# Kernel tuning notes

Hardware: AMD Instinct MI355X
Metric: run time of the kernel (lower is better)

## Reference

```python
import jax, jax.numpy as jnp
import numpy as np
import math

DIM = 512
B, T, H, W = 1, 8, 64, 64


def setup_inputs() -> dict:
    key = jax.random.key(0)
    k0, k1, k2 = jax.random.split(key, 3)
    x = jax.random.normal(k0, (B, DIM, T, H, W), dtype=jnp.float32)
    gamma = jnp.ones((DIM,), jnp.float32)                      # RMS_norm gamma (viewed as flat vector)
    w_qkv = jax.random.normal(k1, (3 * DIM, DIM), jnp.float32) * 0.02  # conv1x1 weight (out, in)
    b_qkv = jnp.zeros((3 * DIM,), jnp.float32)
    w_proj = jax.random.normal(k2, (DIM, DIM), jnp.float32) * 0.02     # zero-init in torch; random for a meaningful baseline
    b_proj = jnp.zeros((DIM,), jnp.float32)
    return dict(x=x, gamma=gamma, w_qkv=w_qkv, b_qkv=b_qkv, w_proj=w_proj, b_proj=b_proj)


def reference(x, gamma, w_qkv, b_qkv, w_proj, b_proj):
    b, c, t, h, w = x.shape
    xt = jnp.transpose(x, (0, 2, 3, 4, 1))          # [b, t, h, w, c]
    identity = xt
    y = xt.reshape(b * t, h, w, c)
    # RMS_norm: L2 norm over channels (last dim), clamped, scaled by sqrt(c)*gamma
    norm = jnp.clip(jnp.linalg.norm(y, axis=-1, keepdims=True), 1e-12, None)
    y = y / norm * (c ** 0.5) * gamma
    # 1x1 conv QKV as GEMM over channels
    qkv = jnp.einsum('bhwc,oc->bhwo', y, w_qkv) + b_qkv        # [bt, h, w, 3c]
    qkv = qkv.reshape(b * t, h * w, 1, 3 * c)                  # nh=1 per source rearrange
    q, k, v = jnp.split(qkv, 3, axis=-1)                       # each [bt, hw, 1, c]
    scale = 1.0 / math.sqrt(c)
    # NOTE: hw sits in the batch position (faithful to source); seq len = nh = 1
    attn = jnp.einsum('bsnc,bsmc->bsnm', q, k) * scale         # [bt, hw, 1, 1]
    attn = jax.nn.softmax(attn, axis=-1)                       # trivially 1.0
    o = jnp.einsum('bsnm,bsmc->bsnc', attn, v)                 # == v
    o = o.reshape(b * t, h, w, c)
    o = jnp.einsum('bhwc,oc->bhwo', o, w_proj) + b_proj        # 1x1 proj conv
    o = o.reshape(b, t, h, w, c)
    out = jnp.transpose(o + identity, (0, 4, 1, 2, 3))         # back to [b, c, t, h, w]
    return out
```

## Files before the change

### kernel.cpp

```cpp
#include <hip/hip_runtime.h>

typedef unsigned short ushort_t;
typedef __attribute__((ext_vector_type(8))) short short8;
typedef __attribute__((ext_vector_type(4))) float f32x4;

#define DIMC 512
#define PN   32768
#define SQRTC 22.627416997969522f

__device__ __forceinline__ ushort_t f2bf(float f) {
  unsigned int u = __float_as_uint(f);
  unsigned int r = u + 0x7fffu + ((u >> 16) & 1u);
  return (ushort_t)(r >> 16);
}

__global__ __launch_bounds__(256) void k_cast(const float* __restrict__ a,
                                              ushort_t* __restrict__ b) {
  int i = (blockIdx.x * 256 + threadIdx.x) * 4;
  float4 v = *(const float4*)(a + i);
  ushort_t o[4] = {f2bf(v.x), f2bf(v.y), f2bf(v.z), f2bf(v.w)};
  *(uint2*)(b + i) = *(const uint2*)o;
}

__global__ __launch_bounds__(64) void k_wvt(const float* __restrict__ wqkv,
                                            ushort_t* __restrict__ WvT) {
  int c = blockIdx.x;
  int k8 = threadIdx.x * 8;
  ushort_t tmp[8];
#pragma unroll
  for (int j = 0; j < 8; ++j)
    tmp[j] = f2bf(wqkv[(long)(1024 + k8 + j) * DIMC + c]);
  *(uint4*)(WvT + (long)c * DIMC + k8) = *(const uint4*)tmp;
}

__global__ __launch_bounds__(256) void k_fb(const float* __restrict__ wp,
                                            const float* __restrict__ bqkv,
                                            const float* __restrict__ bproj,
                                            float* __restrict__ fb) {
  int wave = threadIdx.x >> 6;
  int lane = threadIdx.x & 63;
  int o = blockIdx.x * 4 + wave;
  float part = 0.f;
#pragma unroll
  for (int i = 0; i < 8; ++i) {
    int k = lane + i * 64;
    part += wp[o * DIMC + k] * bqkv[1024 + k];
  }
  for (int off = 32; off; off >>= 1) part += __shfl_down(part, off, 64);
  if (lane == 0) fb[o] = part + bproj[o];
}

__global__ __launch_bounds__(256) void k_prep_x(const float* __restrict__ x,
                                                ushort_t* __restrict__ xT,
                                                float* __restrict__ s) {
  __shared__ ushort_t xt[64 * 264];
  __shared__ float red[16 * 64];
  int tid = threadIdx.x;
  long p0 = (long)blockIdx.x * 64;
  int cg = tid >> 4;
  int p4 = (tid & 15) * 4;
  float ss0 = 0.f, ss1 = 0.f, ss2 = 0.f, ss3 = 0.f;
  for (int half = 0; half < 2; ++half) {
    __syncthreads();
#pragma unroll 4
    for (int pass = 0; pass < 16; ++pass) {
      int cl = pass * 16 + cg;
      int c = half * 256 + cl;
      float4 v = *(const float4*)(x + (long)c * PN + p0 + p4);
      xt[(p4 + 0) * 264 + cl] = f2bf(v.x);
      xt[(p4 + 1) * 264 + cl] = f2bf(v.y);
      xt[(p4 + 2) * 264 + cl] = f2bf(v.z);
      xt[(p4 + 3) * 264 + cl] = f2bf(v.w);
      ss0 += v.x * v.x; ss1 += v.y * v.y; ss2 += v.z * v.z; ss3 += v.w * v.w;
    }
    __syncthreads();
#pragma unroll
    for (int i = 0; i < 8; ++i) {
      int chunk = tid + i * 256;
      int r = chunk >> 5;
      int c8 = (chunk & 31) * 8;
      uint4 v = *(const uint4*)(&xt[r * 264 + c8]);
      *(uint4*)(xT + (p0 + r) * DIMC + half * 256 + c8) = v;
    }
  }
  red[cg * 64 + p4 + 0] = ss0;
  red[cg * 64 + p4 + 1] = ss1;
  red[cg * 64 + p4 + 2] = ss2;
  red[cg * 64 + p4 + 3] = ss3;
  __syncthreads();
  if (tid < 64) {
    float t = 0.f;
#pragma unroll
    for (int g = 0; g < 16; ++g) t += red[g * 64 + tid];
    s[p0 + tid] = SQRTC / fmaxf(sqrtf(t), 1e-12f);
  }
}

template <int EPI>
__global__ __launch_bounds__(256) void k_gemm_f(
    const ushort_t* __restrict__ A,
    const ushort_t* __restrict__ BT,
    long Nstr,
    void* __restrict__ Cv,
    const float* __restrict__ gamma,
    const float* __restrict__ xid,
    const float* __restrict__ fb,
    const float* __restrict__ s) {
  __shared__ ushort_t As[128 * 64];
  __shared__ ushort_t Bs[128 * 64];
  int tid = threadIdx.x;
  int p0 = blockIdx.x * 128;
  int o0 = blockIdx.y * 128;
  int wave = tid >> 6, lane = tid & 63;
  int wo = (wave & 1) * 64, wp = (wave >> 1) * 64;
  int q = lane >> 4, ln = lane & 15;

  f32x4 zero = {0.f, 0.f, 0.f, 0.f};
  f32x4 acc[4][4];
#pragma unroll
  for (int i = 0; i < 4; ++i)
#pragma unroll
    for (int j = 0; j < 4; ++j) acc[i][j] = zero;

  int sr = tid >> 3;
  int sc = tid & 7;
  const ushort_t* Ag = A + (long)(o0 + sr) * DIMC + sc * 8;
  const ushort_t* Bg = BT + (long)(p0 + sr) * DIMC + sc * 8;

  for (int kc = 0; kc < DIMC; kc += 64) {
    __syncthreads();
#pragma unroll
    for (int it = 0; it < 4; ++it) {
      int r = sr + it * 32;
      uint4 va = *(const uint4*)(Ag + (long)it * 32 * DIMC + kc);
      uint4 vb = *(const uint4*)(Bg + (long)it * 32 * DIMC + kc);
      int sw = ((sc ^ (r & 7)) * 8);
      *(uint4*)(&As[r * 64 + sw]) = va;
      *(uint4*)(&Bs[r * 64 + sw]) = vb;
    }
    __syncthreads();
#pragma unroll
    for (int ks = 0; ks < 2; ++ks) {
      int cch = ks * 4 + q;
      short8 af[4], bf[4];
#pragma unroll
      for (int mi = 0; mi < 4; ++mi) {
        int row = wo + mi * 16 + ln;
        af[mi] = *(const short8*)(&As[row * 64 + ((cch ^ (row & 7)) * 8)]);
      }
#pragma unroll
      for (int ni = 0; ni < 4; ++ni) {
        int row = wp + ni * 16 + ln;
        bf[ni] = *(const short8*)(&Bs[row * 64 + ((cch ^ (row & 7)) * 8)]);
      }
#pragma unroll
      for (int mi = 0; mi < 4; ++mi)
#pragma unroll
        for (int ni = 0; ni < 4; ++ni)
          acc[mi][ni] = __builtin_amdgcn_mfma_f32_16x16x32_bf16(af[mi], bf[ni], acc[mi][ni], 0, 0, 0);
    }
  }

#pragma unroll
  for (int mi = 0; mi < 4; ++mi) {
    int obase = o0 + wo + mi * 16 + q * 4;
#pragma unroll
    for (int ni = 0; ni < 4; ++ni) {
      int p = p0 + wp + ni * 16 + ln;
      if (EPI == 0) {
        ushort_t* C = (ushort_t*)Cv;
        float g = gamma[p];
#pragma unroll
        for (int r = 0; r < 4; ++r)
          C[(long)(obase + r) * Nstr + p] = f2bf(acc[mi][ni][r] * g);
      } else {
        float* C = (float*)Cv;
        float sv = s[p];
#pragma unroll
        for (int r = 0; r < 4; ++r) {
          int o = obase + r;
          C[(long)o * Nstr + p] = xid[(long)o * Nstr + p] + fb[o] + sv * acc[mi][ni][r];
        }
      }
    }
  }
}

extern "C" void kernel_launch(void* const* d_in, const int* in_sizes, int n_in,
                              void* d_out, int out_size, void* d_ws, size_t ws_size,
                              hipStream_t stream) {
  const float* x     = (const float*)d_in[0];
  const float* gamma = (const float*)d_in[1];
  const float* wqkv  = (const float*)d_in[2];
  const float* bqkv  = (const float*)d_in[3];
  const float* wproj = (const float*)d_in[4];
  const float* bproj = (const float*)d_in[5];

  char* ws = (char*)d_ws;
  ushort_t* Mp  = (ushort_t*)(ws);
  ushort_t* wpb = (ushort_t*)(ws + 524288);
  ushort_t* WvT = (ushort_t*)(ws + 1048576);
  float*    fb  = (float*)(ws + 1572864);
  float*    s   = (float*)(ws + 1576960);
  ushort_t* xT  = (ushort_t*)(ws + 2097152);

  k_cast<<<dim3(256), dim3(256), 0, stream>>>(wproj, wpb);
  k_wvt<<<dim3(512), dim3(64), 0, stream>>>(wqkv, WvT);
  k_fb<<<dim3(128), dim3(256), 0, stream>>>(wproj, bqkv, bproj, fb);
  k_prep_x<<<dim3(512), dim3(256), 0, stream>>>(x, xT, s);
  k_gemm_f<0><<<dim3(4, 4), dim3(256), 0, stream>>>(
      wpb, WvT, 512, Mp, gamma, nullptr, nullptr, nullptr);
  k_gemm_f<1><<<dim3(256, 4), dim3(256), 0, stream>>>(
      Mp, xT, PN, d_out, nullptr, x, fb, s);
}
```

Before: 176.6 us.

## Merge prep kernels into one launch, use direct global-to-LDS loads, vectorize epilogue

Combines the weight cast, Wv transpose, bias fold, x transpose/norm and the small weight GEMM into one heterogeneous kernel that branches on block index. This cuts the six launches down to two. The main GEMM now loads tiles with global_load_lds, writing swizzled rows straight into shared memory. Its epilogue is staged through LDS so the residual read and output write use float4 along the pixel dimension instead of scalar strided stores. In exchange, the small GEMM reads its B operand from LDS with scalar gathers, and the epilogue adds extra block-wide barriers.

```diff
diff --git a/kernel.cpp b/kernel.cpp
--- a/kernel.cpp
+++ b/kernel.cpp
@@ -13,101 +13,169 @@
   unsigned int r = u + 0x7fffu + ((u >> 16) & 1u);
   return (ushort_t)(r >> 16);
 }
-
-__global__ __launch_bounds__(256) void k_cast(const float* __restrict__ a,
-                                              ushort_t* __restrict__ b) {
-  int i = (blockIdx.x * 256 + threadIdx.x) * 4;
-  float4 v = *(const float4*)(a + i);
-  ushort_t o[4] = {f2bf(v.x), f2bf(v.y), f2bf(v.z), f2bf(v.w)};
-  *(uint2*)(b + i) = *(const uint2*)o;
-}
-
-__global__ __launch_bounds__(64) void k_wvt(const float* __restrict__ wqkv,
-                                            ushort_t* __restrict__ WvT) {
-  int c = blockIdx.x;
-  int k8 = threadIdx.x * 8;
-  ushort_t tmp[8];
-#pragma unroll
-  for (int j = 0; j < 8; ++j)
-    tmp[j] = f2bf(wqkv[(long)(1024 + k8 + j) * DIMC + c]);
-  *(uint4*)(WvT + (long)c * DIMC + k8) = *(const uint4*)tmp;
-}
-
-__global__ __launch_bounds__(256) void k_fb(const float* __restrict__ wp,
-                                            const float* __restrict__ bqkv,
-                                            const float* __restrict__ bproj,
-                                            float* __restrict__ fb) {
-  int wave = threadIdx.x >> 6;
-  int lane = threadIdx.x & 63;
-  int o = blockIdx.x * 4 + wave;
-  float part = 0.f;
-#pragma unroll
-  for (int i = 0; i < 8; ++i) {
-    int k = lane + i * 64;
-    part += wp[o * DIMC + k] * bqkv[1024 + k];
+__device__ __forceinline__ unsigned int pack2(float lo, float hi) {
+  return ((unsigned int)f2bf(hi) << 16) | (unsigned int)f2bf(lo);
+}
+
+typedef __attribute__((address_space(1))) unsigned int glb_u32;
+typedef __attribute__((address_space(3))) unsigned int lds_u32;
+__device__ __forceinline__ void gl_lds16(const ushort_t* g, ushort_t* l) {
+  __builtin_amdgcn_global_load_lds((const glb_u32*)(g), (lds_u32*)(l), 16, 0, 0);
+}
+
+__global__ __launch_bounds__(256) void k_prep(
+    const float* __restrict__ x, const float* __restrict__ gamma,
+    const float* __restrict__ wqkv, const float* __restrict__ bqkv,
+    const float* __restrict__ wproj, const float* __restrict__ bproj,
+    ushort_t* __restrict__ Mp, float* __restrict__ fb,
+    float* __restrict__ s, ushort_t* __restrict__ xT) {
+  __shared__ ushort_t uls[18944];
+  int bb = blockIdx.x;
+  int tid = threadIdx.x;
+
+  if (bb < 512) {
+    ushort_t* xt = uls;
+    float* red = (float*)(uls + 16896);
+    long p0 = (long)bb * 64;
+    int cg = tid >> 4;
+    int p4 = (tid & 15) * 4;
+    float ss0 = 0.f, ss1 = 0.f, ss2 = 0.f, ss3 = 0.f;
+    for (int half = 0; half < 2; ++half) {
+      __syncthreads();
+#pragma unroll 4
+      for (int pass = 0; pass < 16; ++pass) {
+        int cl = pass * 16 + cg;
+        int c = half * 256 + cl;
+        float4 v = *(const float4*)(x + (long)c * PN + p0 + p4);
+        xt[(p4 + 0) * 264 + cl] = f2bf(v.x);
+        xt[(p4 + 1) * 264 + cl] = f2bf(v.y);
+        xt[(p4 + 2) * 264 + cl] = f2bf(v.z);
+        xt[(p4 + 3) * 264 + cl] = f2bf(v.w);
+        ss0 += v.x * v.x; ss1 += v.y * v.y; ss2 += v.z * v.z; ss3 += v.w * v.w;
+      }
+      __syncthreads();
+#pragma unroll
+      for (int i = 0; i < 8; ++i) {
+        int chunk = tid + i * 256;
+        int r = chunk >> 5;
+        int c8 = (chunk & 31) * 8;
+        uint4 v = *(const uint4*)(&xt[r * 264 + c8]);
+        *(uint4*)(xT + (p0 + r) * DIMC + half * 256 + c8) = v;
+      }
+    }
+    red[cg * 64 + p4 + 0] = ss0;
+    red[cg * 64 + p4 + 1] = ss1;
+    red[cg * 64 + p4 + 2] = ss2;
+    red[cg * 64 + p4 + 3] = ss3;
+    __syncthreads();
+    if (tid < 64) {
+      float t = 0.f;
+#pragma unroll
+      for (int g = 0; g < 16; ++g) t += red[g * 64 + tid];
+      s[p0 + tid] = SQRTC / fmaxf(sqrtf(t), 1e-12f);
+    }
+
+  } else if (bb < 528) {
+    ushort_t* As = uls;
+    ushort_t* Bs = uls + 8192;
+    const float* A = wproj;
+    const float* B = wqkv + 1024 * DIMC;
+    int bidx = bb - 512;
+    int p0 = (bidx & 3) * 128;
+    int o0 = (bidx >> 2) * 128;
+    int wave = tid >> 6, lane = tid & 63;
+    int wo = (wave & 1) * 64, wp = (wave >> 1) * 64;
+    int q = lane >> 4, ln = lane & 15;
+    f32x4 zero = {0.f, 0.f, 0.f, 0.f};
+    f32x4 acc[4][4];
+#pragma unroll
+    for (int i = 0; i < 4; ++i)
+#pragma unroll
+      for (int j = 0; j < 4; ++j) acc[i][j] = zero;
+    int ar = tid >> 3, ac = (tid & 7) * 8;
+    int br = tid >> 4, bc = (tid & 15) * 8;
+    for (int kc = 0; kc < DIMC; kc += 64) {
+      __syncthreads();
+#pragma unroll
+      for (int it = 0; it < 4; ++it) {
+        int r = ar + it * 32;
+        const float* ap = A + (long)(o0 + r) * DIMC + kc + ac;
+        float4 a0 = *(const float4*)ap;
+        float4 a1 = *(const float4*)(ap + 4);
+        uint4 wa;
+        wa.x = pack2(a0.x, a0.y); wa.y = pack2(a0.z, a0.w);
+        wa.z = pack2(a1.x, a1.y); wa.w = pack2(a1.z, a1.w);
+        *(uint4*)(&As[r * 64 + ac]) = wa;
+        int kr = br + it * 16;
+        const float* bp = B + (long)(kc + kr) * DIMC + p0 + bc;
+        float4 b0 = *(const float4*)bp;
+        float4 b1 = *(const float4*)(bp + 4);
+        uint4 wb;
+        wb.x = pack2(b0.x, b0.y); wb.y = pack2(b0.z, b0.w);
+        wb.z = pack2(b1.x, b1.y); wb.w = pack2(b1.z, b1.w);
+        *(uint4*)(&Bs[kr * 128 + bc]) = wb;
+      }
+      __syncthreads();
+#pragma unroll
+      for (int ks = 0; ks < 2; ++ks) {
+        int kb = ks * 32 + q * 8;
+        short8 af[4], bfr[4];
+#pragma unroll
+        for (int mi = 0; mi < 4; ++mi)
+          af[mi] = *(const short8*)(&As[(wo + mi * 16 + ln) * 64 + kb]);
+#pragma unroll
+        for (int ni = 0; ni < 4; ++ni) {
+          int pl = wp + ni * 16 + ln;
+          short8 t;
+#pragma unroll
+          for (int j = 0; j < 8; ++j) t[j] = (short)Bs[(kb + j) * 128 + pl];
+          bfr[ni] = t;
+        }
+#pragma unroll
+        for (int mi = 0; mi < 4; ++mi)
+#pragma unroll
+          for (int ni = 0; ni < 4; ++ni)
+            acc[mi][ni] = __builtin_amdgcn_mfma_f32_16x16x32_bf16(af[mi], bfr[ni], acc[mi][ni], 0, 0, 0);
+      }
+    }
+#pragma unroll
+    for (int mi = 0; mi < 4; ++mi) {
+      int obase = o0 + wo + mi * 16 + q * 4;
+#pragma unroll
+      for (int ni = 0; ni < 4; ++ni) {
+        int p = p0 + wp + ni * 16 + ln;
+        float g = gamma[p];
+#pragma unroll
+        for (int r = 0; r < 4; ++r)
+          Mp[(long)(obase + r) * DIMC + p] = f2bf(acc[mi][ni][r] * g);
+      }
+    }
+
+  } else {
+    int wave = tid >> 6;
+    int lane = tid & 63;
+    int o = (bb - 528) * 4 + wave;
+    float part = 0.f;
+#pragma unroll
+    for (int i = 0; i < 8; ++i) {
+      int k = lane + i * 64;
+      part += wproj[o * DIMC + k] * bqkv[1024 + k];
+    }
+    for (int off = 32; off; off >>= 1) part += __shfl_down(part, off, 64);
+    if (lane == 0) fb[o] = part + bproj[o];
   }
-  for (int off = 32; off; off >>= 1) part += __shfl_down(part, off, 64);
-  if (lane == 0) fb[o] = part + bproj[o];
-}
-
-__global__ __launch_bounds__(256) void k_prep_x(const float* __restrict__ x,
-                                                ushort_t* __restrict__ xT,
-                                                float* __restrict__ s) {
-  __shared__ ushort_t xt[64 * 264];
-  __shared__ float red[16 * 64];
-  int tid = threadIdx.x;
-  long p0 = (long)blockIdx.x * 64;
-  int cg = tid >> 4;
-  int p4 = (tid & 15) * 4;
-  float ss0 = 0.f, ss1 = 0.f, ss2 = 0.f, ss3 = 0.f;
-  for (int half = 0; half < 2; ++half) {
-    __syncthreads();
-#pragma unroll 4
-    for (int pass = 0; pass < 16; ++pass) {
-      int cl = pass * 16 + cg;
-      int c = half * 256 + cl;
-      float4 v = *(const float4*)(x + (long)c * PN + p0 + p4);
-      xt[(p4 + 0) * 264 + cl] = f2bf(v.x);
-      xt[(p4 + 1) * 264 + cl] = f2bf(v.y);
-      xt[(p4 + 2) * 264 + cl] = f2bf(v.z);
-      xt[(p4 + 3) * 264 + cl] = f2bf(v.w);
-      ss0 += v.x * v.x; ss1 += v.y * v.y; ss2 += v.z * v.z; ss3 += v.w * v.w;
-    }
-    __syncthreads();
-#pragma unroll
-    for (int i = 0; i < 8; ++i) {
-      int chunk = tid + i * 256;
-      int r = chunk >> 5;
-      int c8 = (chunk & 31) * 8;
-      uint4 v = *(const uint4*)(&xt[r * 264 + c8]);
-      *(uint4*)(xT + (p0 + r) * DIMC + half * 256 + c8) = v;
-    }
-  }
-  red[cg * 64 + p4 + 0] = ss0;
-  red[cg * 64 + p4 + 1] = ss1;
-  red[cg * 64 + p4 + 2] = ss2;
-  red[cg * 64 + p4 + 3] = ss3;
-  __syncthreads();
-  if (tid < 64) {
-    float t = 0.f;
-#pragma unroll
-    for (int g = 0; g < 16; ++g) t += red[g * 64 + tid];
-    s[p0 + tid] = SQRTC / fmaxf(sqrtf(t), 1e-12f);
-  }
-}
-
-template <int EPI>
-__global__ __launch_bounds__(256) void k_gemm_f(
+}
+
+__global__ __launch_bounds__(256) void k_main(
     const ushort_t* __restrict__ A,
     const ushort_t* __restrict__ BT,
-    long Nstr,
-    void* __restrict__ Cv,
-    const float* __restrict__ gamma,
+    float* __restrict__ C,
     const float* __restrict__ xid,
     const float* __restrict__ fb,
     const float* __restrict__ s) {
-  __shared__ ushort_t As[128 * 64];
-  __shared__ ushort_t Bs[128 * 64];
+  __shared__ ushort_t smem[2 * 128 * 64];
+  ushort_t* As = smem;
+  ushort_t* Bs = smem + 128 * 64;
   int tid = threadIdx.x;
   int p0 = blockIdx.x * 128;
   int o0 = blockIdx.y * 128;
@@ -122,22 +190,19 @@
 #pragma unroll
     for (int j = 0; j < 4; ++j) acc[i][j] = zero;
 
-  int sr = tid >> 3;
-  int sc = tid & 7;
-  const ushort_t* Ag = A + (long)(o0 + sr) * DIMC + sc * 8;
-  const ushort_t* Bg = BT + (long)(p0 + sr) * DIMC + sc * 8;
+  int lr = lane >> 3;
+  int lc = lane & 7;
+  int csw = lc ^ lr;
 
   for (int kc = 0; kc < DIMC; kc += 64) {
     __syncthreads();
 #pragma unroll
     for (int it = 0; it < 4; ++it) {
-      int r = sr + it * 32;
-      uint4 va = *(const uint4*)(Ag + (long)it * 32 * DIMC + kc);
-      uint4 vb = *(const uint4*)(Bg + (long)it * 32 * DIMC + kc);
-      int sw = ((sc ^ (r & 7)) * 8);
-      *(uint4*)(&As[r * 64 + sw]) = va;
-      *(uint4*)(&Bs[r * 64 + sw]) = vb;
-    }
+      int rb = (it * 4 + wave) * 8;
+      gl_lds16(A  + (long)(o0 + rb + lr) * DIMC + kc + csw * 8, &As[rb * 64]);
+      gl_lds16(BT + (long)(p0 + rb + lr) * DIMC + kc + csw * 8, &Bs[rb * 64]);
+    }
+    asm volatile("s_waitcnt vmcnt(0)" ::: "memory");
     __syncthreads();
 #pragma unroll
     for (int ks = 0; ks < 2; ++ks) {
@@ -161,27 +226,31 @@
     }
   }
 
+  float* scr = (float*)smem + wave * 1088;
+  float4 s4 = *(const float4*)(s + p0 + wp + ln * 4);
 #pragma unroll
   for (int mi = 0; mi < 4; ++mi) {
-    int obase = o0 + wo + mi * 16 + q * 4;
-#pragma unroll
-    for (int ni = 0; ni < 4; ++ni) {
-      int p = p0 + wp + ni * 16 + ln;
-      if (EPI == 0) {
-        ushort_t* C = (ushort_t*)Cv;
-        float g = gamma[p];
-#pragma unroll
-        for (int r = 0; r < 4; ++r)
-          C[(long)(obase + r) * Nstr + p] = f2bf(acc[mi][ni][r] * g);
-      } else {
-        float* C = (float*)Cv;
-        float sv = s[p];
-#pragma unroll
-        for (int r = 0; r < 4; ++r) {
-          int o = obase + r;
-          C[(long)o * Nstr + p] = xid[(long)o * Nstr + p] + fb[o] + sv * acc[mi][ni][r];
-        }
-      }
+    __syncthreads();
+#pragma unroll
+    for (int ni = 0; ni < 4; ++ni)
+#pragma unroll
+      for (int r = 0; r < 4; ++r)
+        scr[(q * 4 + r) * 68 + ni * 16 + ln] = acc[mi][ni][r];
+    __syncthreads();
+    int ob = o0 + wo + mi * 16 + q;
+    int p = p0 + wp + ln * 4;
+#pragma unroll
+    for (int j = 0; j < 4; ++j) {
+      int o = ob + j * 4;
+      float4 d = *(const float4*)(&scr[(q + j * 4) * 68 + ln * 4]);
+      float4 xv = *(const float4*)(xid + (long)o * PN + p);
+      float fbv = fb[o];
+      float4 ov;
+      ov.x = xv.x + fbv + s4.x * d.x;
+      ov.y = xv.y + fbv + s4.y * d.y;
+      ov.z = xv.z + fbv + s4.z * d.z;
+      ov.w = xv.w + fbv + s4.w * d.w;
+      *(float4*)(C + (long)o * PN + p) = ov;
     }
   }
 }
@@ -197,19 +266,12 @@
   const float* bproj = (const float*)d_in[5];
 
   char* ws = (char*)d_ws;
-  ushort_t* Mp  = (ushort_t*)(ws);
-  ushort_t* wpb = (ushort_t*)(ws + 524288);
-  ushort_t* WvT = (ushort_t*)(ws + 1048576);
-  float*    fb  = (float*)(ws + 1572864);
-  float*    s   = (float*)(ws + 1576960);
-  ushort_t* xT  = (ushort_t*)(ws + 2097152);
-
-  k_cast<<<dim3(256), dim3(256), 0, stream>>>(wproj, wpb);
-  k_wvt<<<dim3(512), dim3(64), 0, stream>>>(wqkv, WvT);
-  k_fb<<<dim3(128), dim3(256), 0, stream>>>(wproj, bqkv, bproj, fb);
-  k_prep_x<<<dim3(512), dim3(256), 0, stream>>>(x, xT, s);
-  k_gemm_f<0><<<dim3(4, 4), dim3(256), 0, stream>>>(
-      wpb, WvT, 512, Mp, gamma, nullptr, nullptr, nullptr);
-  k_gemm_f<1><<<dim3(256, 4), dim3(256), 0, stream>>>(
-      Mp, xT, PN, d_out, nullptr, x, fb, s);
-}
+  ushort_t* Mp = (ushort_t*)(ws);
+  float*    fb = (float*)(ws + 524288);
+  float*    s  = (float*)(ws + 526336);
+  ushort_t* xT = (ushort_t*)(ws + 2097152);
+
+  k_prep<<<dim3(656), dim3(256), 0, stream>>>(x, gamma, wqkv, bqkv, wproj, bproj,
+                                              Mp, fb, s, xT);
+  k_main<<<dim3(256, 4), dim3(256), 0, stream>>>(Mp, xT, (float*)d_out, x, fb, s);
+}
```

Measured after the change: 184.9 us. 4.7% more time.
